# Optimization experiments

Measured on AMD Instinct MI355X. Metric: run time of the kernel, lower is better.

The kernel has to match this reference:

```python
import jax, jax.numpy as jnp
import numpy as np

N_NODES = 50000
N_EDGES = 800000
IN_DIM, HID_DIM, OUT_DIM = 256, 128, 64


def setup_inputs() -> dict:
    key = jax.random.key(0)
    ks = jax.random.split(key, 8)
    x = jax.random.normal(ks[0], (N_NODES, IN_DIM), dtype=jnp.float32)
    edge_index = jax.random.randint(ks[1], (2, N_EDGES), 0, N_NODES, dtype=jnp.int64)
    # Glorot-ish init for GCNConv weights (PyG stores weight as [in, out] in lin layer; math is x @ W)
    def glorot(k, shape):
        lim = (6.0 / (shape[0] + shape[1])) ** 0.5
        return jax.random.uniform(k, shape, jnp.float32, -lim, lim)
    return {
        "x": x,
        "edge_index": edge_index,
        "W1": glorot(ks[2], (IN_DIM, HID_DIM)), "b1": jnp.zeros((HID_DIM,), jnp.float32),
        "W2": glorot(ks[3], (HID_DIM, HID_DIM)), "b2": jnp.zeros((HID_DIM,), jnp.float32),
        "W3": glorot(ks[4], (HID_DIM, OUT_DIM)), "b3": jnp.zeros((OUT_DIM,), jnp.float32),
    }


def _gcn_norm(edge_index, n):
    # PyG gcn_norm with add_self_loops=True: A_hat = D^-1/2 (A + I) D^-1/2
    loops = jnp.arange(n, dtype=edge_index.dtype)
    src = jnp.concatenate([edge_index[0], loops])  # [E+N]
    dst = jnp.concatenate([edge_index[1], loops])  # [E+N]
    deg = jax.ops.segment_sum(jnp.ones_like(dst, dtype=jnp.float32), dst, num_segments=n)
    dinv = jnp.where(deg > 0, deg ** -0.5, 0.0)
    norm = dinv[src] * dinv[dst]  # [E+N]
    return src, dst, norm


def _gcn_layer(x, W, b, src, dst, norm, n):
    h = x @ W                                  # [N, F_out] transform first (GCNConv order)
    m = h[src] * norm[:, None]                 # edge-gather + normalize
    agg = jax.ops.segment_sum(m, dst, num_segments=n)  # scatter-add aggregation
    return agg + b


def reference(x, edge_index, W1, b1, W2, b2, W3, b3):
    n = x.shape[0]
    src, dst, norm = _gcn_norm(edge_index, n)
    h = jax.nn.relu(_gcn_layer(x, W1, b1, src, dst, norm, n))
    h = jax.nn.relu(_gcn_layer(h, W2, b2, src, dst, norm, n))
    h = jax.nn.relu(_gcn_layer(h, W3, b3, src, dst, norm, n))
    return h
```

## Files before the change

kernel.cpp:

```cpp
#include <hip/hip_runtime.h>
#include <math.h>

typedef _Float16 half8v __attribute__((ext_vector_type(8)));
typedef float    f32x4  __attribute__((ext_vector_type(4)));

#define DSTR 16


__global__ void deg_pos_kernel(const int* __restrict__ dst, int* __restrict__ deg,
                               int* __restrict__ pos, int E) {
    int i = blockIdx.x * blockDim.x + threadIdx.x;
    if (i < E) pos[i] = atomicAdd(&deg[(size_t)dst[i] * DSTR], 1);
}

__global__ __launch_bounds__(256) void scan1_kernel(const int* __restrict__ deg,
                                                    int* __restrict__ row_ptr,
                                                    int* __restrict__ partial,
                                                    float* __restrict__ dinv, int n) {
    __shared__ int s[256];
    int tid = threadIdx.x;
    int i = blockIdx.x * 256 + tid;
    int dg = (i < n) ? deg[(size_t)i * DSTR] : 0;
    if (i < n) dinv[i] = 1.0f / sqrtf((float)(dg + 1));
    int v = (i < n) ? ((dg + 4) & ~3) : 0;
    s[tid] = v;
    __syncthreads();
    #pragma unroll
    for (int off = 1; off < 256; off <<= 1) {
        int t = (tid >= off) ? s[tid - off] : 0;
        __syncthreads();
        s[tid] += t;
        __syncthreads();
    }
    if (i < n) row_ptr[i + 1] = s[tid];
    if (tid == 255) partial[blockIdx.x] = s[255];
}

__global__ __launch_bounds__(256) void scan2_kernel(int* __restrict__ partial, int nb) {
    __shared__ int s[256];
    int tid = threadIdx.x;
    int v = (tid < nb) ? partial[tid] : 0;
    s[tid] = v;
    __syncthreads();
    #pragma unroll
    for (int off = 1; off < 256; off <<= 1) {
        int t = (tid >= off) ? s[tid - off] : 0;
        __syncthreads();
        s[tid] += t;
        __syncthreads();
    }
    if (tid < nb) partial[tid] = s[tid] - v;
}

__global__ void scan3_kernel(const int* __restrict__ partial, int* __restrict__ row_ptr, int n) {
    int i = blockIdx.x * blockDim.x + threadIdx.x;
    if (i == 0) row_ptr[0] = 0;
    if (i < n) row_ptr[i + 1] += partial[i >> 8];
}

__global__ void fill_kernel(const int* __restrict__ ei, const int* __restrict__ pos,
                            const int* __restrict__ deg, const float* __restrict__ dinv,
                            const int* __restrict__ row_ptr, unsigned* __restrict__ csr,
                            int E, int n) {
    int idx = blockIdx.x * blockDim.x + threadIdx.x;
    int s, d, slot;
    if (idx < E)          { s = ei[idx]; d = ei[E + idx]; slot = pos[idx]; }
    else if (idx < E + n) { s = d = idx - E; slot = deg[(size_t)d * DSTR]; }
    else if (idx < E + n + 3 * n) {
        int p = idx - E - n;
        int dd = p / 3, pi = p - dd * 3;
        int dg = deg[(size_t)dd * DSTR];
        int real = dg + 1;
        int padded = (dg + 4) & ~3;
        if (pi < padded - real) csr[row_ptr[dd] + real + pi] = 0u;
        return;
    } else return;
    float w = dinv[s] * dinv[d];
    _Float16 wh = (_Float16)w;
    union { _Float16 h; unsigned short u; } cv; cv.h = wh;
    csr[row_ptr[d] + slot] = (unsigned)s | ((unsigned)cv.u << 16);
}

__global__ void wcvt_kernel(const float* __restrict__ W1, _Float16* __restrict__ Bt1,
                            const float* __restrict__ W2, _Float16* __restrict__ Bt2,
                            const float* __restrict__ W3, _Float16* __restrict__ Bt3) {
    int i = blockIdx.x * blockDim.x + threadIdx.x;
    if (i < 256 * 128) {
        int k = i % 256, n = i / 256;
        Bt1[i] = (_Float16)W1[(size_t)k * 128 + n];
    } else if (i < 256 * 128 + 128 * 128) {
        int j = i - 256 * 128;
        int k = j % 128, n = j / 128;
        Bt2[j] = (_Float16)W2[(size_t)k * 128 + n];
    } else if (i < 256 * 128 + 128 * 128 + 128 * 64) {
        int j = i - 256 * 128 - 128 * 128;
        int k = j % 128, n = j / 128;
        Bt3[j] = (_Float16)W3[(size_t)k * 64 + n];
    }
}

template <typename TA, int K, int TNv>
__global__ __launch_bounds__(256) void mfma_gemm_kernel(const TA* __restrict__ A,
                                                        const _Float16* __restrict__ Bt,
                                                        _Float16* __restrict__ C,
                                                        int M) {
    constexpr int NF = TNv / 16;
    constexpr int KP = K + 8;
    constexpr int CHUNKS = (TNv * (K / 8)) / 256;
    __shared__ _Float16 Bs[TNv * KP];

    int tid = threadIdx.x;
    #pragma unroll
    for (int i = 0; i < CHUNKS; ++i) {
        int id = tid + i * 256;
        int n  = id / (K / 8);
        int k8 = (id % (K / 8)) * 8;
        *(half8v*)(&Bs[n * KP + k8]) = *(const half8v*)(Bt + (size_t)n * K + k8);
    }
    __syncthreads();

    int lane = tid & 63;
    int wave = tid >> 6;
    int r  = lane & 15;
    int kg = lane >> 4;
    int row0 = blockIdx.x * 128 + wave * 32;

    f32x4 acc[2][NF];
    #pragma unroll
    for (int mf = 0; mf < 2; ++mf)
        #pragma unroll
        for (int nf = 0; nf < NF; ++nf)
            acc[mf][nf] = (f32x4){0.f, 0.f, 0.f, 0.f};

    int rowA0 = row0 + r;      if (rowA0 > M - 1) rowA0 = M - 1;
    int rowA1 = row0 + 16 + r; if (rowA1 > M - 1) rowA1 = M - 1;
    const TA* pa0 = A + (size_t)rowA0 * K + kg * 8;
    const TA* pa1 = A + (size_t)rowA1 * K + kg * 8;

    #pragma unroll
    for (int kc = 0; kc < K; kc += 32) {
        half8v a0, a1;
        if constexpr (__is_same(TA, float)) {
            float4 l0 = *(const float4*)(pa0 + kc);
            float4 h0 = *(const float4*)(pa0 + kc + 4);
            float4 l1 = *(const float4*)(pa1 + kc);
            float4 h1 = *(const float4*)(pa1 + kc + 4);
            a0[0] = (_Float16)l0.x; a0[1] = (_Float16)l0.y; a0[2] = (_Float16)l0.z; a0[3] = (_Float16)l0.w;
            a0[4] = (_Float16)h0.x; a0[5] = (_Float16)h0.y; a0[6] = (_Float16)h0.z; a0[7] = (_Float16)h0.w;
            a1[0] = (_Float16)l1.x; a1[1] = (_Float16)l1.y; a1[2] = (_Float16)l1.z; a1[3] = (_Float16)l1.w;
            a1[4] = (_Float16)h1.x; a1[5] = (_Float16)h1.y; a1[6] = (_Float16)h1.z; a1[7] = (_Float16)h1.w;
        } else {
            a0 = *(const half8v*)(pa0 + kc);
            a1 = *(const half8v*)(pa1 + kc);
        }
        #pragma unroll
        for (int nf = 0; nf < NF; ++nf) {
            half8v b = *(const half8v*)(&Bs[(nf * 16 + r) * KP + kc + kg * 8]);
            acc[0][nf] = __builtin_amdgcn_mfma_f32_16x16x32_f16(a0, b, acc[0][nf], 0, 0, 0);
            acc[1][nf] = __builtin_amdgcn_mfma_f32_16x16x32_f16(a1, b, acc[1][nf], 0, 0, 0);
        }
    }

    #pragma unroll
    for (int mf = 0; mf < 2; ++mf) {
        #pragma unroll
        for (int j = 0; j < 4; ++j) {
            int row = row0 + mf * 16 + kg * 4 + j;
            if (row < M) {
                #pragma unroll
                for (int nf = 0; nf < NF; ++nf)
                    C[(size_t)row * TNv + nf * 16 + r] = (_Float16)acc[mf][nf][j];
            }
        }
    }
}

template <int F, typename TOut>
__global__ __launch_bounds__(256) void spmm_kernel(const _Float16* __restrict__ H,
                                                   const int* __restrict__ row_ptr,
                                                   const unsigned* __restrict__ csr,
                                                   const float* __restrict__ bias,
                                                   TOut* __restrict__ out,
                                                   int n_nodes) {
    constexpr int LPR = F / 8;
    constexpr int RPW = 64 / LPR;
    constexpr int U16 = 16 / RPW;
    constexpr int U8  = 8 / RPW;
    int wave = threadIdx.x >> 6;
    int lane = threadIdx.x & 63;
    int node = (blockIdx.x << 2) + wave;
    if (node >= n_nodes) return;

    int h  = lane / LPR;
    int fi = (lane % LPR) * 8;
    const _Float16* Hf = H + fi;

    int e0 = row_ptr[node];
    int e1 = row_ptr[node + 1];

    float acc[U16][8];
    #pragma unroll
    for (int i = 0; i < U16; ++i)
        #pragma unroll
        for (int j = 0; j < 8; ++j) acc[i][j] = 0.f;

    auto unpack_w = [](unsigned pk) -> float {
        union { unsigned short u; _Float16 h; } cv;
        cv.u = (unsigned short)(pk >> 16);
        return (float)cv.h;
    };

    int e = e0;
    for (; e + 16 <= e1; e += 16) {
        unsigned pk[U16];
        #pragma unroll
        for (int i = 0; i < U16; ++i) pk[i] = csr[e + i * RPW + h];
        #pragma unroll
        for (int i = 0; i < U16; ++i) {
            half8v v = *(const half8v*)(Hf + (size_t)(pk[i] & 0xFFFFu) * F);
            float w = unpack_w(pk[i]);
            #pragma unroll
            for (int j = 0; j < 8; ++j) acc[i][j] = fmaf(w, (float)v[j], acc[i][j]);
        }
    }
    if (e + 8 <= e1) {
        unsigned pk[U8];
        #pragma unroll
        for (int i = 0; i < U8; ++i) pk[i] = csr[e + i * RPW + h];
        #pragma unroll
        for (int i = 0; i < U8; ++i) {
            half8v v = *(const half8v*)(Hf + (size_t)(pk[i] & 0xFFFFu) * F);
            float w = unpack_w(pk[i]);
            #pragma unroll
            for (int j = 0; j < 8; ++j) acc[i][j] = fmaf(w, (float)v[j], acc[i][j]);
        }
        e += 8;
    }
    if (e < e1) {
        unsigned pk = (RPW == 4 || h < 4) ? csr[e + h] : 0u;
        half8v v = *(const half8v*)(Hf + (size_t)(pk & 0xFFFFu) * F);
        float w = unpack_w(pk);
        #pragma unroll
        for (int j = 0; j < 8; ++j) acc[0][j] = fmaf(w, (float)v[j], acc[0][j]);
    }

    float t[8];
    #pragma unroll
    for (int j = 0; j < 8; ++j) {
        t[j] = acc[0][j];
        #pragma unroll
        for (int i = 1; i < U16; ++i) t[j] += acc[i][j];
    }
    #pragma unroll
    for (int off = LPR; off < 64; off <<= 1)
        #pragma unroll
        for (int j = 0; j < 8; ++j) t[j] += __shfl_xor(t[j], off);

    if (h == 0) {
        float4 bl = *(const float4*)(bias + fi);
        float4 bh = *(const float4*)(bias + fi + 4);
        float o[8];
        o[0] = fmaxf(t[0] + bl.x, 0.f); o[1] = fmaxf(t[1] + bl.y, 0.f);
        o[2] = fmaxf(t[2] + bl.z, 0.f); o[3] = fmaxf(t[3] + bl.w, 0.f);
        o[4] = fmaxf(t[4] + bh.x, 0.f); o[5] = fmaxf(t[5] + bh.y, 0.f);
        o[6] = fmaxf(t[6] + bh.z, 0.f); o[7] = fmaxf(t[7] + bh.w, 0.f);
        if constexpr (__is_same(TOut, _Float16)) {
            half8v hv;
            #pragma unroll
            for (int j = 0; j < 8; ++j) hv[j] = (_Float16)o[j];
            *(half8v*)(out + (size_t)node * F + fi) = hv;
        } else {
            *(float4*)(out + (size_t)node * F + fi)     = make_float4(o[0], o[1], o[2], o[3]);
            *(float4*)(out + (size_t)node * F + fi + 4) = make_float4(o[4], o[5], o[6], o[7]);
        }
    }
}


extern "C" void kernel_launch(void* const* d_in, const int* in_sizes, int n_in,
                              void* d_out, int out_size, void* d_ws, size_t ws_size,
                              hipStream_t stream) {
    const float* x  = (const float*)d_in[0];
    const int*   ei = (const int*)d_in[1];
    const float* W1 = (const float*)d_in[2];
    const float* b1 = (const float*)d_in[3];
    const float* W2 = (const float*)d_in[4];
    const float* b2 = (const float*)d_in[5];
    const float* W3 = (const float*)d_in[6];
    const float* b3 = (const float*)d_in[7];

    const int IN_DIM = 256, HID = 128, OUT = 64;
    int n_nodes = in_sizes[0] / IN_DIM;
    int n_edges = in_sizes[1] / 2;
    int nnz_cap = n_edges + 4 * n_nodes;

    char* ws = (char*)d_ws;
    size_t off = 0;
    auto carve = [&](size_t bytes) { void* p = ws + off; off += (bytes + 255) & ~(size_t)255; return p; };
    _Float16* Hbuf = (_Float16*)carve((size_t)n_nodes * HID * sizeof(_Float16));
    _Float16* Bbuf = (_Float16*)carve((size_t)n_nodes * HID * sizeof(_Float16));
    _Float16* Bt1  = (_Float16*)carve((size_t)IN_DIM * HID * sizeof(_Float16));
    _Float16* Bt2  = (_Float16*)carve((size_t)HID * HID * sizeof(_Float16));
    _Float16* Bt3  = (_Float16*)carve((size_t)HID * OUT * sizeof(_Float16));
    int*   deg     = (int*)carve((size_t)n_nodes * DSTR * sizeof(int));
    float* dinv    = (float*)carve((size_t)n_nodes * sizeof(float));
    int*   row_ptr = (int*)carve((size_t)(n_nodes + 1) * sizeof(int));
    int*   pos     = (int*)carve((size_t)n_edges * sizeof(int));
    int*   partial = (int*)carve(256 * sizeof(int));
    unsigned* csr  = (unsigned*)carve((size_t)nnz_cap * sizeof(unsigned));
    if (off > ws_size) return;

    float* out = (float*)d_out;

    const int B = 256;
    int nb = (n_nodes + 255) / 256;

    hipMemsetAsync(deg, 0, (size_t)n_nodes * DSTR * sizeof(int), stream);
    deg_pos_kernel<<<(n_edges + B - 1) / B, B, 0, stream>>>(ei + n_edges, deg, pos, n_edges);
    scan1_kernel<<<nb, 256, 0, stream>>>(deg, row_ptr, partial, dinv, n_nodes);
    scan2_kernel<<<1, 256, 0, stream>>>(partial, nb);
    scan3_kernel<<<(n_nodes + B - 1) / B, B, 0, stream>>>(partial, row_ptr, n_nodes);
    fill_kernel<<<(n_edges + 4 * n_nodes + B - 1) / B, B, 0, stream>>>(ei, pos, deg, dinv,
                                                                       row_ptr, csr, n_edges, n_nodes);
    int wtot = IN_DIM * HID + HID * HID + HID * OUT;
    wcvt_kernel<<<(wtot + B - 1) / B, B, 0, stream>>>(W1, Bt1, W2, Bt2, W3, Bt3);

    int spmm_grid = (n_nodes + 3) / 4;
    int gemm_grid = (n_nodes + 127) / 128;

    mfma_gemm_kernel<float, 256, 128><<<gemm_grid, 256, 0, stream>>>(x, Bt1, Hbuf, n_nodes);
    spmm_kernel<128, _Float16><<<spmm_grid, 256, 0, stream>>>(Hbuf, row_ptr, csr, b1, Bbuf, n_nodes);
    mfma_gemm_kernel<_Float16, 128, 128><<<gemm_grid, 256, 0, stream>>>(Bbuf, Bt2, Hbuf, n_nodes);
    spmm_kernel<128, _Float16><<<spmm_grid, 256, 0, stream>>>(Hbuf, row_ptr, csr, b2, Bbuf, n_nodes);
    mfma_gemm_kernel<_Float16, 128, 64><<<gemm_grid, 256, 0, stream>>>(Bbuf, Bt3, Hbuf, n_nodes);
    spmm_kernel<64, float><<<spmm_grid, 256, 0, stream>>>(Hbuf, row_ptr, csr, b3, out, n_nodes);
}
```

Before: 191.7 us.

## Fuse graph preprocessing into one cooperative kernel with grid syncs

Replaces the memset and six preprocessing kernels (degree count, three-phase scan, CSR fill, weight conversion) with a single cooperative kernel of 1024 blocks that separates the phases with grid-wide barriers. This is meant to remove per-launch overhead and the inter-kernel gaps on the stream. The cost is grid-stride loops over fewer threads and several grid.sync barriers, and a cooperative launch can fail if 1024 blocks cannot all be co-resident.

```diff
diff --git a/kernel.cpp b/kernel.cpp
--- a/kernel.cpp
+++ b/kernel.cpp
@@ -1,5 +1,8 @@
 #include <hip/hip_runtime.h>
+#include <hip/hip_cooperative_groups.h>
 #include <math.h>
+
+namespace cg = cooperative_groups;
 
 typedef _Float16 half8v __attribute__((ext_vector_type(8)));
 typedef float    f32x4  __attribute__((ext_vector_type(4)));
@@ -7,95 +10,92 @@
 #define DSTR 16
 
 
-__global__ void deg_pos_kernel(const int* __restrict__ dst, int* __restrict__ deg,
-                               int* __restrict__ pos, int E) {
-    int i = blockIdx.x * blockDim.x + threadIdx.x;
-    if (i < E) pos[i] = atomicAdd(&deg[(size_t)dst[i] * DSTR], 1);
-}
-
-__global__ __launch_bounds__(256) void scan1_kernel(const int* __restrict__ deg,
-                                                    int* __restrict__ row_ptr,
-                                                    int* __restrict__ partial,
-                                                    float* __restrict__ dinv, int n) {
+__global__ __launch_bounds__(256) void preproc_kernel(
+    const int* __restrict__ ei, int E, int n,
+    int* __restrict__ deg, int* __restrict__ pos, int* __restrict__ row_ptr,
+    int* __restrict__ partial, float* __restrict__ dinv, unsigned* __restrict__ csr,
+    const float* __restrict__ W1, const float* __restrict__ W2,
+    const float* __restrict__ W3,
+    _Float16* __restrict__ Bt1, _Float16* __restrict__ Bt2,
+    _Float16* __restrict__ Bt3)
+{
+    cg::grid_group grid = cg::this_grid();
     __shared__ int s[256];
-    int tid = threadIdx.x;
-    int i = blockIdx.x * 256 + tid;
-    int dg = (i < n) ? deg[(size_t)i * DSTR] : 0;
-    if (i < n) dinv[i] = 1.0f / sqrtf((float)(dg + 1));
-    int v = (i < n) ? ((dg + 4) & ~3) : 0;
-    s[tid] = v;
-    __syncthreads();
-    #pragma unroll
-    for (int off = 1; off < 256; off <<= 1) {
-        int t = (tid >= off) ? s[tid - off] : 0;
+    const int ltid = threadIdx.x;
+    const int tid  = blockIdx.x * 256 + ltid;
+    const int nth  = gridDim.x * 256;
+    const int* dstp = ei + E;
+
+    for (int i = tid; i < n; i += nth) deg[(size_t)i * DSTR] = 0;
+    const int w1e = 256 * 128, w2e = w1e + 128 * 128, w3e = w2e + 128 * 64;
+    for (int i = tid; i < w3e; i += nth) {
+        if (i < w1e)      { int k = i & 255, nn = i >> 8;           Bt1[i] = (_Float16)W1[(size_t)k * 128 + nn]; }
+        else if (i < w2e) { int j = i - w1e; int k = j & 127, nn = j >> 7; Bt2[j] = (_Float16)W2[(size_t)k * 128 + nn]; }
+        else              { int j = i - w2e; int k = j & 127, nn = j >> 7; Bt3[j] = (_Float16)W3[(size_t)k * 64 + nn]; }
+    }
+    grid.sync();
+
+    for (int i = tid; i < E; i += nth)
+        pos[i] = atomicAdd(&deg[(size_t)dstp[i] * DSTR], 1);
+    grid.sync();
+
+    int nb = (n + 255) >> 8;
+    for (int c = blockIdx.x; c < nb; c += gridDim.x) {
+        int i = (c << 8) + ltid;
+        int dg = (i < n) ? deg[(size_t)i * DSTR] : 0;
+        if (i < n) dinv[i] = 1.0f / sqrtf((float)(dg + 1));
+        int v = (i < n) ? ((dg + 4) & ~3) : 0;
+        s[ltid] = v;
         __syncthreads();
-        s[tid] += t;
+        #pragma unroll
+        for (int off = 1; off < 256; off <<= 1) {
+            int t = (ltid >= off) ? s[ltid - off] : 0;
+            __syncthreads();
+            s[ltid] += t;
+            __syncthreads();
+        }
+        if (i < n) row_ptr[i + 1] = s[ltid];
+        if (ltid == 255) partial[c] = s[255];
         __syncthreads();
     }
-    if (i < n) row_ptr[i + 1] = s[tid];
-    if (tid == 255) partial[blockIdx.x] = s[255];
-}
-
-__global__ __launch_bounds__(256) void scan2_kernel(int* __restrict__ partial, int nb) {
-    __shared__ int s[256];
-    int tid = threadIdx.x;
-    int v = (tid < nb) ? partial[tid] : 0;
-    s[tid] = v;
-    __syncthreads();
-    #pragma unroll
-    for (int off = 1; off < 256; off <<= 1) {
-        int t = (tid >= off) ? s[tid - off] : 0;
+    grid.sync();
+
+    if (blockIdx.x == 0) {
+        int v = (ltid < nb) ? partial[ltid] : 0;
+        s[ltid] = v;
         __syncthreads();
-        s[tid] += t;
-        __syncthreads();
-    }
-    if (tid < nb) partial[tid] = s[tid] - v;
-}
-
-__global__ void scan3_kernel(const int* __restrict__ partial, int* __restrict__ row_ptr, int n) {
-    int i = blockIdx.x * blockDim.x + threadIdx.x;
-    if (i == 0) row_ptr[0] = 0;
-    if (i < n) row_ptr[i + 1] += partial[i >> 8];
-}
-
-__global__ void fill_kernel(const int* __restrict__ ei, const int* __restrict__ pos,
-                            const int* __restrict__ deg, const float* __restrict__ dinv,
-                            const int* __restrict__ row_ptr, unsigned* __restrict__ csr,
-                            int E, int n) {
-    int idx = blockIdx.x * blockDim.x + threadIdx.x;
-    int s, d, slot;
-    if (idx < E)          { s = ei[idx]; d = ei[E + idx]; slot = pos[idx]; }
-    else if (idx < E + n) { s = d = idx - E; slot = deg[(size_t)d * DSTR]; }
-    else if (idx < E + n + 3 * n) {
-        int p = idx - E - n;
-        int dd = p / 3, pi = p - dd * 3;
-        int dg = deg[(size_t)dd * DSTR];
-        int real = dg + 1;
-        int padded = (dg + 4) & ~3;
-        if (pi < padded - real) csr[row_ptr[dd] + real + pi] = 0u;
-        return;
-    } else return;
-    float w = dinv[s] * dinv[d];
-    _Float16 wh = (_Float16)w;
-    union { _Float16 h; unsigned short u; } cv; cv.h = wh;
-    csr[row_ptr[d] + slot] = (unsigned)s | ((unsigned)cv.u << 16);
-}
-
-__global__ void wcvt_kernel(const float* __restrict__ W1, _Float16* __restrict__ Bt1,
-                            const float* __restrict__ W2, _Float16* __restrict__ Bt2,
-                            const float* __restrict__ W3, _Float16* __restrict__ Bt3) {
-    int i = blockIdx.x * blockDim.x + threadIdx.x;
-    if (i < 256 * 128) {
-        int k = i % 256, n = i / 256;
-        Bt1[i] = (_Float16)W1[(size_t)k * 128 + n];
-    } else if (i < 256 * 128 + 128 * 128) {
-        int j = i - 256 * 128;
-        int k = j % 128, n = j / 128;
-        Bt2[j] = (_Float16)W2[(size_t)k * 128 + n];
-    } else if (i < 256 * 128 + 128 * 128 + 128 * 64) {
-        int j = i - 256 * 128 - 128 * 128;
-        int k = j % 128, n = j / 128;
-        Bt3[j] = (_Float16)W3[(size_t)k * 64 + n];
+        #pragma unroll
+        for (int off = 1; off < 256; off <<= 1) {
+            int t = (ltid >= off) ? s[ltid - off] : 0;
+            __syncthreads();
+            s[ltid] += t;
+            __syncthreads();
+        }
+        if (ltid < nb) partial[ltid] = s[ltid] - v;
+    }
+    grid.sync();
+
+    if (tid == 0) row_ptr[0] = 0;
+    for (int i = tid; i < n; i += nth) row_ptr[i + 1] += partial[i >> 8];
+    grid.sync();
+
+    int total = E + n + 3 * n;
+    for (int idx = tid; idx < total; idx += nth) {
+        int sn, d, slot;
+        if (idx < E)          { sn = ei[idx]; d = dstp[idx]; slot = pos[idx]; }
+        else if (idx < E + n) { sn = d = idx - E; slot = deg[(size_t)d * DSTR]; }
+        else {
+            int p = idx - E - n;
+            int dd = p / 3, pi = p - dd * 3;
+            int dg = deg[(size_t)dd * DSTR];
+            int real = dg + 1;
+            int padded = (dg + 4) & ~3;
+            if (pi < padded - real) csr[row_ptr[dd] + real + pi] = 0u;
+            continue;
+        }
+        float w = dinv[sn] * dinv[d];
+        union { _Float16 h; unsigned short u; } cv; cv.h = (_Float16)w;
+        csr[row_ptr[d] + slot] = (unsigned)sn | ((unsigned)cv.u << 16);
     }
 }
 
@@ -312,18 +312,17 @@
 
     float* out = (float*)d_out;
 
-    const int B = 256;
-    int nb = (n_nodes + 255) / 256;
-
-    hipMemsetAsync(deg, 0, (size_t)n_nodes * DSTR * sizeof(int), stream);
-    deg_pos_kernel<<<(n_edges + B - 1) / B, B, 0, stream>>>(ei + n_edges, deg, pos, n_edges);
-    scan1_kernel<<<nb, 256, 0, stream>>>(deg, row_ptr, partial, dinv, n_nodes);
-    scan2_kernel<<<1, 256, 0, stream>>>(partial, nb);
-    scan3_kernel<<<(n_nodes + B - 1) / B, B, 0, stream>>>(partial, row_ptr, n_nodes);
-    fill_kernel<<<(n_edges + 4 * n_nodes + B - 1) / B, B, 0, stream>>>(ei, pos, deg, dinv,
-                                                                       row_ptr, csr, n_edges, n_nodes);
-    int wtot = IN_DIM * HID + HID * HID + HID * OUT;
-    wcvt_kernel<<<(wtot + B - 1) / B, B, 0, stream>>>(W1, Bt1, W2, Bt2, W3, Bt3);
+    {
+        void* kargs[] = {
+            (void*)&ei, (void*)&n_edges, (void*)&n_nodes,
+            (void*)&deg, (void*)&pos, (void*)&row_ptr, (void*)&partial,
+            (void*)&dinv, (void*)&csr,
+            (void*)&W1, (void*)&W2, (void*)&W3,
+            (void*)&Bt1, (void*)&Bt2, (void*)&Bt3,
+        };
+        hipLaunchCooperativeKernel((const void*)preproc_kernel,
+                                   dim3(1024), dim3(256), kargs, 0, stream);
+    }
 
     int spmm_grid = (n_nodes + 3) / 4;
     int gemm_grid = (n_nodes + 127) / 128;
```

Result: slower. 692.4 us (+261.2%).
